# Optimization experiments

Measured on AMD Instinct MI355X. Metric: run time of the kernel, lower is better.

The kernel has to match this reference:

```python
import jax, jax.numpy as jnp
import numpy as np

N_ATOMS = 100000
N_PAIRS = 100000  # undirected bonds; directed edges = 2*N_PAIRS
ATOM_DIM, BOND_DIM, HIDDEN = 133, 14, 512
T_STEPS = 3


def setup_inputs() -> dict:
    rng = np.random.default_rng(0)
    # Build directed edges as reversed pairs: edge 2i = (a,b), edge 2i+1 = (b,a).
    a = rng.integers(0, N_ATOMS, size=N_PAIRS)
    b = rng.integers(0, N_ATOMS, size=N_PAIRS)
    src = np.empty(2 * N_PAIRS, dtype=np.int64)
    dst = np.empty(2 * N_PAIRS, dtype=np.int64)
    src[0::2], dst[0::2] = a, b
    src[1::2], dst[1::2] = b, a
    edge_index = jnp.asarray(np.stack([src, dst], axis=0))
    rev_edge_index = jnp.asarray(np.arange(2 * N_PAIRS, dtype=np.int64) ^ 1)
    atom_batch = jnp.asarray(np.sort(rng.integers(0, 256, size=N_ATOMS)).astype(np.int64))

    key = jax.random.key(0)
    ks = jax.random.split(key, 8)
    V = jax.random.normal(ks[0], (N_ATOMS, ATOM_DIM), dtype=jnp.float32)
    E = jax.random.normal(ks[1], (2 * N_PAIRS, BOND_DIM), dtype=jnp.float32)
    weight = jax.random.uniform(ks[2], (2 * N_PAIRS,), dtype=jnp.float32)
    s = 0.05
    W_i = jax.random.normal(ks[3], (HIDDEN, ATOM_DIM + BOND_DIM), dtype=jnp.float32) * s
    W_h = jax.random.normal(ks[4], (HIDDEN, HIDDEN), dtype=jnp.float32) * s
    W_o = jax.random.normal(ks[5], (HIDDEN, ATOM_DIM + HIDDEN), dtype=jnp.float32) * s
    b_o = jax.random.normal(ks[6], (HIDDEN,), dtype=jnp.float32) * s
    return {"V": V, "E": E, "edge_index": edge_index, "rev_edge_index": rev_edge_index,
            "atom_batch": atom_batch, "weight": weight,
            "W_i": W_i, "W_h": W_h, "W_o": W_o, "b_o": b_o}


def reference(V, E, edge_index, rev_edge_index, atom_batch, weight, W_i, W_h, W_o, b_o):
    n_atoms = V.shape[0]
    src, dest = edge_index[0], edge_index[1]
    # edge init: h0 = ReLU(W_i [V[src] ; E])
    inp = jnp.concatenate([V[src], E], axis=1)          # [E, atom+bond]
    h0 = jax.nn.relu(inp @ W_i.T)                        # [E, H]
    h = h0
    for _ in range(T_STEPS):
        wh = h * weight[:, None]                          # [E, H]
        m_to_atom = jax.ops.segment_sum(wh, dest, num_segments=n_atoms)  # [N, H]
        m = m_to_atom[src] - weight[rev_edge_index][:, None] * h[rev_edge_index]
        h = jax.nn.relu(m @ W_h.T + h0)
    m_final = jax.ops.segment_sum(h, dest, num_segments=n_atoms)  # [N, H]
    atom_in = jnp.concatenate([V, m_final], axis=1)      # [N, atom+H]
    h_atom = jax.nn.relu(atom_in @ W_o.T + b_o)          # [N, H]
    return (h_atom, atom_batch, h)
```

## Files before the change

kernel.cpp:

```cpp
#include <hip/hip_runtime.h>

typedef __attribute__((ext_vector_type(8))) short short8;
typedef __attribute__((ext_vector_type(4))) float f32x4;

#define N_ATOMS_C 100000
#define N_EDGES_C 200000
#define ATOM_DIM_C 133
#define BOND_DIM_C 14
#define HID_C 512

#define KT0 5
#define KT1 16
#define KT2 21

__device__ __forceinline__ unsigned short bf16_rne(float f) {
  unsigned int u = __float_as_uint(f);
  unsigned int r = (u + 0x7fffu + ((u >> 16) & 1u)) >> 16;
  return (unsigned short)r;
}
__device__ __forceinline__ float bf16_to_f(unsigned short h) {
  return __uint_as_float(((unsigned int)h) << 16);
}

template <int K, int KTILES>
__global__ __launch_bounds__(256) void prep_w(const float* __restrict__ W,
                                              short8* __restrict__ hi,
                                              short8* __restrict__ lo) {
  const int idx = blockIdx.x * 256 + threadIdx.x;
  if (idx >= 2 * KTILES * 1024) return;
  const int nb = idx / (KTILES * 1024);
  const int rem = idx - nb * (KTILES * 1024);
  const int kt = rem >> 10;
  const int c = rem & 1023;
  const int l = c & 63;
  const int n = nb * 256 + ((c >> 6) << 4) + (l & 15);
  const int k0 = kt * 32 + ((l >> 4) << 3);
  short8 h8, l8;
#pragma unroll
  for (int j = 0; j < 8; ++j) {
    const int k = k0 + j;
    const float f = (k < K) ? W[(size_t)n * K + k] : 0.f;
    const unsigned short hb = bf16_rne(f);
    h8[j] = (short)hb;
    l8[j] = (short)bf16_rne(f - bf16_to_f(hb));
  }
  hi[idx] = h8;
  lo[idx] = l8;
}

template <int MODE, int KTILES, bool SCATTER>
__global__ __launch_bounds__(256, 3) void mfma_gemm(
    const short8* __restrict__ wHi, const short8* __restrict__ wLo,
    const float* __restrict__ in0, const float* __restrict__ in1,
    const float* __restrict__ addv, const float* __restrict__ wrev,
    const int* __restrict__ srcp, const int* __restrict__ dstp,
    const float* __restrict__ wscat, float* __restrict__ C,
    float* __restrict__ m2a, int M) {
  __shared__ short8 Ahi[256], Alo[256];
  __shared__ short8 Bhi[1024], Blo[1024];
  __shared__ int sSrc[64], sDst[64];
  __shared__ float sWe[64], sWrev[64];

  const int tid = threadIdx.x;
  const int nwg = gridDim.x;
  const int qq = nwg >> 3, rr = nwg & 7;
  const int x = blockIdx.x & 7, o = blockIdx.x >> 3;
  const int wg = (x < rr ? x * (qq + 1) : rr * (qq + 1) + (x - rr) * qq) + o;
  const int cb = wg & 1, rb = wg >> 1;
  const int bm0 = rb * 64, bn0 = cb * 256;

  if (tid < 64) {
    const int e = bm0 + tid;
    const int ec = e < M ? e : M - 1;
    if (MODE != 2) sSrc[tid] = srcp[ec];
    if (SCATTER) {
      sDst[tid] = dstp[ec];
      sWe[tid] = wscat ? wscat[ec] : 1.f;
    }
    if (MODE == 1) sWrev[tid] = wrev[ec ^ 1];
  }
  __syncthreads();

  const int w = tid >> 6, lane = tid & 63;
  const int r = tid >> 2, kc = tid & 3;
  const int arow = bm0 + r;
  const int arc = arow < M ? arow : M - 1;

  const float* p0 = nullptr;
  const float* p1 = nullptr;
  float wr_ = 0.f;
  if (MODE == 0) {
    p0 = in0 + (size_t)sSrc[r] * ATOM_DIM_C;
    p1 = in1 + (size_t)arc * BOND_DIM_C;
  } else if (MODE == 1) {
    p0 = in0 + ((size_t)sSrc[r] << 9);
    p1 = in1 + ((size_t)(arc ^ 1) << 9);
    wr_ = sWrev[r];
  } else {
    p0 = in0 + (size_t)arc * ATOM_DIM_C;
    p1 = in1 + ((size_t)arc << 9);
  }

  f32x4 acc[4][4];
#pragma unroll
  for (int i = 0; i < 4; ++i)
#pragma unroll
    for (int j = 0; j < 4; ++j) acc[i][j] = f32x4{0.f, 0.f, 0.f, 0.f};

  const short8* gHi = wHi + (size_t)cb * KTILES * 1024;
  const short8* gLo = wLo + (size_t)cb * KTILES * 1024;
  const int aslot = ((r >> 4) << 6) | (r & 15) | (kc << 4);

  for (int kt = 0; kt < KTILES; ++kt) {
    const int k0 = kt * 32 + kc * 8;
    float v[8];
    if (MODE == 1) {
      const float4 m0 = *(const float4*)(p0 + k0);
      const float4 m1 = *(const float4*)(p0 + k0 + 4);
      const float4 g0 = *(const float4*)(p1 + k0);
      const float4 g1 = *(const float4*)(p1 + k0 + 4);
      v[0] = m0.x - wr_ * g0.x; v[1] = m0.y - wr_ * g0.y;
      v[2] = m0.z - wr_ * g0.z; v[3] = m0.w - wr_ * g0.w;
      v[4] = m1.x - wr_ * g1.x; v[5] = m1.y - wr_ * g1.y;
      v[6] = m1.z - wr_ * g1.z; v[7] = m1.w - wr_ * g1.w;
    } else {
#pragma unroll
      for (int j = 0; j < 8; ++j) {
        const int k = k0 + j;
        float f = 0.f;
        if (k < ATOM_DIM_C) f = p0[k];
        else if (k < (MODE == 0 ? 147 : 645)) f = p1[k - ATOM_DIM_C];
        v[j] = f;
      }
    }
    short8 h8, l8;
#pragma unroll
    for (int j = 0; j < 8; ++j) {
      const unsigned short hb = bf16_rne(v[j]);
      h8[j] = (short)hb;
      l8[j] = (short)bf16_rne(v[j] - bf16_to_f(hb));
    }
    __syncthreads();
    Ahi[aslot] = h8;
    Alo[aslot] = l8;
    const int kb = kt << 10;
#pragma unroll
    for (int p = 0; p < 4; ++p) {
      const int cc = p * 256 + tid;
      Bhi[cc] = gHi[kb + cc];
      Blo[cc] = gLo[kb + cc];
    }
    __syncthreads();
    short8 bh[4], bl[4];
#pragma unroll
    for (int nj = 0; nj < 4; ++nj) {
      bh[nj] = Bhi[(((w << 2) + nj) << 6) + lane];
      bl[nj] = Blo[(((w << 2) + nj) << 6) + lane];
    }
#pragma unroll
    for (int mi = 0; mi < 4; ++mi) {
      const short8 ah = Ahi[(mi << 6) + lane];
      const short8 al = Alo[(mi << 6) + lane];
#pragma unroll
      for (int nj = 0; nj < 4; ++nj) {
        acc[mi][nj] = __builtin_amdgcn_mfma_f32_16x16x32_bf16(ah, bh[nj], acc[mi][nj], 0, 0, 0);
        acc[mi][nj] = __builtin_amdgcn_mfma_f32_16x16x32_bf16(al, bh[nj], acc[mi][nj], 0, 0, 0);
        acc[mi][nj] = __builtin_amdgcn_mfma_f32_16x16x32_bf16(ah, bl[nj], acc[mi][nj], 0, 0, 0);
      }
    }
  }

  const int lq = lane >> 4, lc = lane & 15;
#pragma unroll
  for (int mi = 0; mi < 4; ++mi) {
#pragma unroll
    for (int nj = 0; nj < 4; ++nj) {
      const int ccol = bn0 + (((w << 2) + nj) << 4) + lc;
      const f32x4 a = acc[mi][nj];
#pragma unroll
      for (int q2 = 0; q2 < 4; ++q2) {
        const int rloc = (mi << 4) + (lq << 2) + q2;
        const int row = bm0 + rloc;
        if (row < M) {
          float xv = a[q2];
          if (MODE == 1) xv += addv[((size_t)row << 9) + ccol];
          if (MODE == 2) xv += addv[ccol];
          xv = fmaxf(xv, 0.f);
          C[((size_t)row << 9) + ccol] = xv;
          if (SCATTER) atomicAdd(m2a + ((size_t)sDst[rloc] << 9) + ccol, sWe[rloc] * xv);
        }
      }
    }
  }
}

__global__ __launch_bounds__(256) void batch_copy_kernel(const int* __restrict__ b,
                                                         float* __restrict__ o) {
  const int i = blockIdx.x * 256 + threadIdx.x;
  if (i < N_ATOMS_C) o[i] = (float)b[i];
}

extern "C" void kernel_launch(void* const* d_in, const int* in_sizes, int n_in,
                              void* d_out, int out_size, void* d_ws, size_t ws_size,
                              hipStream_t stream) {
  const float* V = (const float*)d_in[0];
  const float* E = (const float*)d_in[1];
  const int* edge_index = (const int*)d_in[2];
  const int* batch = (const int*)d_in[4];
  const float* weight = (const float*)d_in[5];
  const float* W_i = (const float*)d_in[6];
  const float* W_h = (const float*)d_in[7];
  const float* W_o = (const float*)d_in[8];
  const float* b_o = (const float*)d_in[9];

  const int* src = edge_index;
  const int* dst = edge_index + N_EDGES_C;

  float* ws = (float*)d_ws;
  float* h0 = ws;
  float* hA = h0 + (size_t)N_EDGES_C * HID_C;
  float* mA = hA + (size_t)N_EDGES_C * HID_C;
  float* mB = mA + (size_t)N_ATOMS_C * HID_C;
  short8* wiHi = (short8*)(mB + (size_t)N_ATOMS_C * HID_C);
  short8* wiLo = wiHi + 2 * KT0 * 1024;
  short8* whHi = wiLo + 2 * KT0 * 1024;
  short8* whLo = whHi + 2 * KT1 * 1024;
  short8* woHi = whLo + 2 * KT1 * 1024;
  short8* woLo = woHi + 2 * KT2 * 1024;

  float* out = (float*)d_out;
  float* out_hatom = out;
  float* out_batch = out + (size_t)N_ATOMS_C * HID_C;
  float* out_h = out_batch + N_ATOMS_C;

  prep_w<147, KT0><<<(2 * KT0 * 1024 + 255) / 256, 256, 0, stream>>>(W_i, wiHi, wiLo);
  prep_w<512, KT1><<<(2 * KT1 * 1024 + 255) / 256, 256, 0, stream>>>(W_h, whHi, whLo);
  prep_w<645, KT2><<<(2 * KT2 * 1024 + 255) / 256, 256, 0, stream>>>(W_o, woHi, woLo);

  const size_t mBytes = (size_t)N_ATOMS_C * HID_C * sizeof(float);
  const int gE = (N_EDGES_C / 64) * 2;
  const int gA = ((N_ATOMS_C + 63) / 64) * 2;

  hipMemsetAsync(mA, 0, mBytes, stream);
  mfma_gemm<0, KT0, true><<<gE, 256, 0, stream>>>(wiHi, wiLo, V, E, nullptr, nullptr,
                                                  src, dst, weight, h0, mA, N_EDGES_C);
  hipMemsetAsync(mB, 0, mBytes, stream);
  mfma_gemm<1, KT1, true><<<gE, 256, 0, stream>>>(whHi, whLo, mA, h0, h0, weight,
                                                  src, dst, weight, out_h, mB, N_EDGES_C);
  hipMemsetAsync(mA, 0, mBytes, stream);
  mfma_gemm<1, KT1, true><<<gE, 256, 0, stream>>>(whHi, whLo, mB, out_h, h0, weight,
                                                  src, dst, weight, hA, mA, N_EDGES_C);
  hipMemsetAsync(mB, 0, mBytes, stream);
  mfma_gemm<1, KT1, true><<<gE, 256, 0, stream>>>(whHi, whLo, mA, hA, h0, weight,
                                                  src, dst, nullptr, out_h, mB, N_EDGES_C);
  mfma_gemm<2, KT2, false><<<gA, 256, 0, stream>>>(woHi, woLo, V, mB, b_o, nullptr,
                                                   nullptr, nullptr, nullptr, out_hatom,
                                                   nullptr, N_ATOMS_C);
  batch_copy_kernel<<<(N_ATOMS_C + 255) / 256, 256, 0, stream>>>(batch, out_batch);
}
```

Before: 4.196 ms.

## Software-pipeline GEMM K-loop with register prefetch and double-buffered A tiles

Restructures the MFMA GEMM main loop into a two-stage software pipeline. Global loads for the A and B tiles two steps ahead are issued into registers, and the A tile is double-buffered in shared memory with one barrier per step. B fragments now go straight from global memory into registers instead of being staged through LDS. The aim is to hide global latency behind the MFMAs and cut LDS traffic and barriers, at the cost of more registers, which is why occupancy is lowered from 3 to 2 waves per SIMD.

```diff
diff --git a/kernel.cpp b/kernel.cpp
--- a/kernel.cpp
+++ b/kernel.cpp
@@ -12,6 +12,8 @@
 #define KT0 5
 #define KT1 16
 #define KT2 21
+
+template <int N> struct IC { static constexpr int v = N; };
 
 __device__ __forceinline__ unsigned short bf16_rne(float f) {
   unsigned int u = __float_as_uint(f);
@@ -49,15 +51,14 @@
 }
 
 template <int MODE, int KTILES, bool SCATTER>
-__global__ __launch_bounds__(256, 3) void mfma_gemm(
+__global__ __launch_bounds__(256, 2) void mfma_gemm(
     const short8* __restrict__ wHi, const short8* __restrict__ wLo,
     const float* __restrict__ in0, const float* __restrict__ in1,
     const float* __restrict__ addv, const float* __restrict__ wrev,
     const int* __restrict__ srcp, const int* __restrict__ dstp,
     const float* __restrict__ wscat, float* __restrict__ C,
     float* __restrict__ m2a, int M) {
-  __shared__ short8 Ahi[256], Alo[256];
-  __shared__ short8 Bhi[1024], Blo[1024];
+  __shared__ short8 Ah[2][256], Al[2][256];
   __shared__ int sSrc[64], sDst[64];
   __shared__ float sWe[64], sWrev[64];
 
@@ -85,6 +86,8 @@
   const int r = tid >> 2, kc = tid & 3;
   const int arow = bm0 + r;
   const int arc = arow < M ? arow : M - 1;
+  const int aslot = ((r >> 4) << 6) | (kc << 4) | (r & 15);
+  constexpr int KTOT = (MODE == 0) ? 147 : 645;
 
   const float* p0 = nullptr;
   const float* p1 = nullptr;
@@ -101,37 +104,64 @@
     p1 = in1 + ((size_t)arc << 9);
   }
 
-  f32x4 acc[4][4];
-#pragma unroll
-  for (int i = 0; i < 4; ++i)
-#pragma unroll
-    for (int j = 0; j < 4; ++j) acc[i][j] = f32x4{0.f, 0.f, 0.f, 0.f};
-
   const short8* gHi = wHi + (size_t)cb * KTILES * 1024;
   const short8* gLo = wLo + (size_t)cb * KTILES * 1024;
-  const int aslot = ((r >> 4) << 6) | (r & 15) | (kc << 4);
-
-  for (int kt = 0; kt < KTILES; ++kt) {
-    const int k0 = kt * 32 + kc * 8;
-    float v[8];
+  const int boff = (w << 8) + lane;
+
+  f32x4 acc[4][4];
+#pragma unroll
+  for (int i = 0; i < 4; ++i)
+#pragma unroll
+    for (int j = 0; j < 4; ++j) acc[i][j] = f32x4{0.f, 0.f, 0.f, 0.f};
+
+  float4 pa0[2], pa1[2], pg0[2], pg1[2];
+  float vA[2][8];
+  short8 pbh[2][4], pbl[2][4];
+
+  auto loadA = [&](auto sc, int t) {
+    constexpr int S = decltype(sc)::v;
+    const int k0 = t * 32 + kc * 8;
     if (MODE == 1) {
-      const float4 m0 = *(const float4*)(p0 + k0);
-      const float4 m1 = *(const float4*)(p0 + k0 + 4);
-      const float4 g0 = *(const float4*)(p1 + k0);
-      const float4 g1 = *(const float4*)(p1 + k0 + 4);
-      v[0] = m0.x - wr_ * g0.x; v[1] = m0.y - wr_ * g0.y;
-      v[2] = m0.z - wr_ * g0.z; v[3] = m0.w - wr_ * g0.w;
-      v[4] = m1.x - wr_ * g1.x; v[5] = m1.y - wr_ * g1.y;
-      v[6] = m1.z - wr_ * g1.z; v[7] = m1.w - wr_ * g1.w;
+      pa0[S] = *(const float4*)(p0 + k0);
+      pa1[S] = *(const float4*)(p0 + k0 + 4);
+      pg0[S] = *(const float4*)(p1 + k0);
+      pg1[S] = *(const float4*)(p1 + k0 + 4);
     } else {
 #pragma unroll
       for (int j = 0; j < 8; ++j) {
         const int k = k0 + j;
         float f = 0.f;
         if (k < ATOM_DIM_C) f = p0[k];
-        else if (k < (MODE == 0 ? 147 : 645)) f = p1[k - ATOM_DIM_C];
-        v[j] = f;
+        else if (k < KTOT) f = p1[k - ATOM_DIM_C];
+        vA[S][j] = f;
       }
+    }
+  };
+  auto loadB = [&](auto sc, int t) {
+    constexpr int S = decltype(sc)::v;
+    const short8* gh = gHi + ((size_t)t << 10) + boff;
+    const short8* gl = gLo + ((size_t)t << 10) + boff;
+#pragma unroll
+    for (int nj = 0; nj < 4; ++nj) {
+      pbh[S][nj] = gh[nj << 6];
+      pbl[S][nj] = gl[nj << 6];
+    }
+  };
+  auto splitW = [&](auto sc, int buf) {
+    constexpr int S = decltype(sc)::v;
+    float v[8];
+    if (MODE == 1) {
+      v[0] = pa0[S].x - wr_ * pg0[S].x;
+      v[1] = pa0[S].y - wr_ * pg0[S].y;
+      v[2] = pa0[S].z - wr_ * pg0[S].z;
+      v[3] = pa0[S].w - wr_ * pg0[S].w;
+      v[4] = pa1[S].x - wr_ * pg1[S].x;
+      v[5] = pa1[S].y - wr_ * pg1[S].y;
+      v[6] = pa1[S].z - wr_ * pg1[S].z;
+      v[7] = pa1[S].w - wr_ * pg1[S].w;
+    } else {
+#pragma unroll
+      for (int j = 0; j < 8; ++j) v[j] = vA[S][j];
     }
     short8 h8, l8;
 #pragma unroll
@@ -140,34 +170,44 @@
       h8[j] = (short)hb;
       l8[j] = (short)bf16_rne(v[j] - bf16_to_f(hb));
     }
+    Ah[buf][aslot] = h8;
+    Al[buf][aslot] = l8;
+  };
+
+  auto stepf = [&](auto cc, int t) {
+    constexpr int CUR = decltype(cc)::v;
+    short8 ah[4], al[4];
+#pragma unroll
+    for (int mi = 0; mi < 4; ++mi) {
+      ah[mi] = Ah[CUR][(mi << 6) + lane];
+      al[mi] = Al[CUR][(mi << 6) + lane];
+    }
+    if (t + 2 < KTILES) loadA(IC<CUR>{}, t + 2);
+#pragma unroll
+    for (int mi = 0; mi < 4; ++mi)
+#pragma unroll
+      for (int nj = 0; nj < 4; ++nj) {
+        acc[mi][nj] = __builtin_amdgcn_mfma_f32_16x16x32_bf16(ah[mi], pbh[CUR][nj], acc[mi][nj], 0, 0, 0);
+        acc[mi][nj] = __builtin_amdgcn_mfma_f32_16x16x32_bf16(al[mi], pbh[CUR][nj], acc[mi][nj], 0, 0, 0);
+        acc[mi][nj] = __builtin_amdgcn_mfma_f32_16x16x32_bf16(ah[mi], pbl[CUR][nj], acc[mi][nj], 0, 0, 0);
+      }
+    if (t + 1 < KTILES) splitW(IC<CUR ^ 1>{}, CUR ^ 1);
+    if (t + 2 < KTILES) loadB(IC<CUR>{}, t + 2);
     __syncthreads();
-    Ahi[aslot] = h8;
-    Alo[aslot] = l8;
-    const int kb = kt << 10;
-#pragma unroll
-    for (int p = 0; p < 4; ++p) {
-      const int cc = p * 256 + tid;
-      Bhi[cc] = gHi[kb + cc];
-      Blo[cc] = gLo[kb + cc];
-    }
-    __syncthreads();
-    short8 bh[4], bl[4];
-#pragma unroll
-    for (int nj = 0; nj < 4; ++nj) {
-      bh[nj] = Bhi[(((w << 2) + nj) << 6) + lane];
-      bl[nj] = Blo[(((w << 2) + nj) << 6) + lane];
-    }
-#pragma unroll
-    for (int mi = 0; mi < 4; ++mi) {
-      const short8 ah = Ahi[(mi << 6) + lane];
-      const short8 al = Alo[(mi << 6) + lane];
-#pragma unroll
-      for (int nj = 0; nj < 4; ++nj) {
-        acc[mi][nj] = __builtin_amdgcn_mfma_f32_16x16x32_bf16(ah, bh[nj], acc[mi][nj], 0, 0, 0);
-        acc[mi][nj] = __builtin_amdgcn_mfma_f32_16x16x32_bf16(al, bh[nj], acc[mi][nj], 0, 0, 0);
-        acc[mi][nj] = __builtin_amdgcn_mfma_f32_16x16x32_bf16(ah, bl[nj], acc[mi][nj], 0, 0, 0);
-      }
-    }
+  };
+
+  loadA(IC<0>{}, 0);
+  loadB(IC<0>{}, 0);
+  splitW(IC<0>{}, 0);
+  if (KTILES > 1) {
+    loadA(IC<1>{}, 1);
+    loadB(IC<1>{}, 1);
+  }
+  __syncthreads();
+
+  for (int t = 0; t < KTILES; t += 2) {
+    stepf(IC<0>{}, t);
+    if (t + 1 < KTILES) stepf(IC<1>{}, t + 1);
   }
 
   const int lq = lane >> 4, lc = lane & 15;
```

Result: slower. 4.492 ms (+7.1%).
